# Kernel optimization log

Hardware: AMD Instinct MI355X
Metric: run time of the kernel (lower is better)

Reference implementation:

```python
import jax, jax.numpy as jnp
import numpy as np
import math

NHID = 256
QDIM = 256
T = 4096
B = 4

def setup_inputs() -> dict:
    key = jax.random.key(0)
    k1, k2, k3, k4 = jax.random.split(key, 4)
    # xavier_uniform with relu gain = sqrt(2)
    gain = math.sqrt(2.0)
    bound = gain * math.sqrt(6.0 / (NHID + QDIM))
    inputs = jax.random.normal(k1, (T, B, NHID), dtype=jnp.float32)
    W_q = jax.random.uniform(k2, (NHID, QDIM), minval=-bound, maxval=bound, dtype=jnp.float32)
    W_k = jax.random.uniform(k3, (NHID, QDIM), minval=-bound, maxval=bound, dtype=jnp.float32)
    W_v = jax.random.uniform(k4, (NHID, QDIM), minval=-bound, maxval=bound, dtype=jnp.float32)
    return {"inputs": inputs, "W_q": W_q, "W_k": W_k, "W_v": W_v}

def reference(inputs, W_q, W_k, W_v):
    # inputs: [T, B, H]. Original loops over time, recomputing attention of the
    # last token against the growing causal prefix. Step 0 emits x0 @ W_v, which
    # equals single-key softmax attention, so the whole thing is causal attention.
    scale = float(int(math.sqrt(QDIM)))  # faithful to int(math.sqrt(d)) in source
    q = jnp.einsum('tbh,hd->tbd', inputs, W_q)
    k = jnp.einsum('tbh,hd->tbd', inputs, W_k)
    v = jnp.einsum('tbh,hd->tbd', inputs, W_v)
    scores = jnp.einsum('ibd,jbd->bij', q, k) / scale  # [B, T, T]
    t = scores.shape[-1]
    causal = jnp.tril(jnp.ones((t, t), dtype=bool))
    scores = jnp.where(causal[None, :, :], scores, -jnp.inf)
    attn = jax.nn.softmax(scores, axis=-1)  # row i = attention_thru_time[i]
    results = jnp.einsum('bij,jbd->ibd', attn, v)  # [T, B, D]
    return results, attn
```

## Files before the change

### kernel.cpp

```cpp
#include <hip/hip_runtime.h>
#include <hip/hip_bf16.h>

#define T_DIM 4096
#define B_DIM 4

typedef unsigned short u16;
typedef __attribute__((ext_vector_type(4))) short s16x4;
typedef __attribute__((ext_vector_type(8))) short short8;
typedef __attribute__((ext_vector_type(8))) __bf16 bf16x8;
typedef __attribute__((ext_vector_type(4))) float f32x4;

static __device__ __forceinline__ u16 f2bf(float f) {
    union { float f; unsigned int u; } v; v.f = f;
    unsigned int u = v.u;
    u += 0x7FFFu + ((u >> 16) & 1u);
    return (u16)(u >> 16);
}

static __device__ __forceinline__ f32x4 mfma_k32(short8 a, short8 b, f32x4 c) {
    return __builtin_amdgcn_mfma_f32_16x16x32_bf16(
        __builtin_bit_cast(bf16x8, a), __builtin_bit_cast(bf16x8, b), c, 0, 0, 0);
}
static __device__ __forceinline__ f32x4 mfma_k16(s16x4 a, s16x4 b, f32x4 c) {
    return __builtin_amdgcn_mfma_f32_16x16x16bf16_1k(a, b, c, 0, 0, 0);
}

__global__ __launch_bounds__(256) void wtrans_kernel(
    const float* __restrict__ Wq, const float* __restrict__ Wk,
    const float* __restrict__ Wv, u16* __restrict__ wT) {
    int idx = blockIdx.x * 256 + threadIdx.x;
    int w   = idx >> 16;
    int rem = idx & 65535;
    int k   = rem >> 8;
    int n   = rem & 255;
    const float* W = (w == 0) ? Wq : (w == 1) ? Wk : Wv;
    wT[w * 65536 + n * 256 + k] = f2bf(W[k * 256 + n]);
}

__global__ __launch_bounds__(256, 4) void proj_kernel(
    const float* __restrict__ X, const u16* __restrict__ wT,
    u16* __restrict__ qf, u16* __restrict__ kf, u16* __restrict__ vfw) {
    const int r0  = blockIdx.x * 16;
    const int wid = threadIdx.x >> 6, lane = threadIdx.x & 63;
    const int lr  = lane & 15, lg = lane >> 4;

    short8 af[8];
    const float* xrow = X + (size_t)(r0 + lr) * 256 + lg * 8;
#pragma unroll
    for (int kc = 0; kc < 8; ++kc) {
        f32x4 xa = *(const f32x4*)(xrow + kc * 32);
        f32x4 xb = *(const f32x4*)(xrow + kc * 32 + 4);
        union { u16 u[8]; short8 v; } t;
#pragma unroll
        for (int e = 0; e < 4; ++e) { t.u[e] = f2bf(xa[e]); t.u[4 + e] = f2bf(xb[e]); }
        af[kc] = t.v;
    }

    for (int w = 0; w < 3; ++w) {
        f32x4 acc[4];
#pragma unroll
        for (int nf = 0; nf < 4; ++nf) acc[nf] = (f32x4){0.f,0.f,0.f,0.f};
        const u16* wbase = wT + w * 65536 + (size_t)(16 * (4 * wid) + lr) * 256 + lg * 8;
#pragma unroll
        for (int kc = 0; kc < 8; ++kc)
#pragma unroll
            for (int nf = 0; nf < 4; ++nf) {
                short8 bfv = *(const short8*)(wbase + nf * 16 * 256 + kc * 32);
                acc[nf] = mfma_k32(af[kc], bfv, acc[nf]);
            }
#pragma unroll
        for (int nf = 0; nf < 4; ++nf)
#pragma unroll
            for (int r = 0; r < 4; ++r) {
                int rg = r0 + 4 * lg + r;
                int t  = rg >> 2, bb = rg & 3;
                int d  = 16 * (4 * wid + nf) + lr;
                u16 val = f2bf(acc[nf][r]);
                if (w < 2) {
                    int tile = t >> 4, lrq = t & 15;
                    int kc = d >> 5, lgq = (d >> 3) & 3, e = d & 7;
                    size_t idx = ((((size_t)bb * 256 + tile) * 8 + kc) * 64
                                  + lrq + 16 * lgq) * 8 + e;
                    if (w == 0) qf[idx] = val; else kf[idx] = val;
                } else {
                    int jt = t >> 6, c = (t >> 4) & 3;
                    int cc = c >> 1, eh = c & 1;
                    int lgv = (t >> 2) & 3, el = t & 3, e = eh * 4 + el;
                    int nfv = d >> 4, lrv = d & 15;
                    size_t idx = (((((size_t)bb * 64 + jt) * 16 + nfv) * 2 + cc) * 64
                                  + lrv + 16 * lgv) * 8 + e;
                    vfw[idx] = val;
                }
            }
    }
}

__global__ __launch_bounds__(512) void attn_kernel(
    const u16* __restrict__ qf, const u16* __restrict__ kf,
    const u16* __restrict__ vfw, float* __restrict__ out) {
    __shared__ float l_sm[32];
    __shared__ float O_sm[32 * 264];

    const int blk = blockIdx.x;
    const int xcd = blk & 7;
    const int b = xcd >> 1, par = xcd & 1;
    const int pair = 2 * (blk >> 3) + par;

    const int tid = threadIdx.x;
    const int wid = tid >> 6, lane = tid & 63;
    const int f = wid >> 2, h = wid & 3;
    const int lr = lane & 15, lg = lane >> 4;

    float* attnO = out + (size_t)T_DIM * B_DIM * 256 + (size_t)b * T_DIM * T_DIM;

    for (int phase = 0; phase < 2; ++phase) {
        const int it = phase ? (127 - pair) : pair;
        const int i0 = it * 32;
        const int irow = i0 + 16 * f + lr;
        const int numJT = it / 2 + 1;

        __syncthreads();
        if (tid < 32) l_sm[tid] = 0.f;
        __syncthreads();

        short8 q8[8];
        const short8* qp = (const short8*)(qf + (((size_t)b * 256 + it * 2 + f) * 8) * 512);
#pragma unroll
        for (int kc = 0; kc < 8; ++kc) q8[kc] = qp[kc * 64 + lane];

        float rs = 0.f;
        for (int jt = 0; jt < numJT; ++jt) {
            const short8* kp = (const short8*)(kf + (((size_t)b * 256 + jt * 4 + h) * 8) * 512);
            f32x4 a = {0.f,0.f,0.f,0.f};
#pragma unroll
            for (int kc = 0; kc < 8; ++kc)
                a = mfma_k32(kp[kc * 64 + lane], q8[kc], a);
            const int j0 = jt * 64 + 16 * h + 4 * lg;
#pragma unroll
            for (int r = 0; r < 4; ++r)
                rs += (j0 + r <= irow) ? __expf(a[r] * 0.0625f) : 0.f;
        }
        rs += __shfl_xor(rs, 16, 64);
        rs += __shfl_xor(rs, 32, 64);
        if (lane < 16) atomicAdd(&l_sm[16 * f + lr], rs);
        __syncthreads();
        const float inv = 1.0f / l_sm[16 * f + lr];

        f32x4 oacc[16];
#pragma unroll
        for (int nf = 0; nf < 16; ++nf) oacc[nf] = (f32x4){0.f,0.f,0.f,0.f};

        for (int jt = 0; jt < numJT; ++jt) {
            const short8* kp = (const short8*)(kf + (((size_t)b * 256 + jt * 4 + h) * 8) * 512);
            f32x4 a = {0.f,0.f,0.f,0.f};
#pragma unroll
            for (int kc = 0; kc < 8; ++kc)
                a = mfma_k32(kp[kc * 64 + lane], q8[kc], a);

            const int j0 = jt * 64 + 16 * h + 4 * lg;
#pragma unroll
            for (int r = 0; r < 4; ++r)
                a[r] = (j0 + r <= irow) ? __expf(a[r] * 0.0625f) * inv : 0.f;
            __builtin_nontemporal_store(a,
                (f32x4*)(attnO + (size_t)irow * T_DIM + j0));

            union { u16 u[4]; s16x4 v; } t;
#pragma unroll
            for (int r = 0; r < 4; ++r) t.u[r] = f2bf(a[r]);
            const s16x4 pk = t.v;

            const u16* vb = vfw + (((size_t)b * 64 + jt) * 32 + (h >> 1)) * 512
                          + (size_t)lane * 8 + (h & 1) * 4;
#pragma unroll
            for (int nf = 0; nf < 16; ++nf) {
                s16x4 vf = *(const s16x4*)(vb + (size_t)nf * 1024);
                oacc[nf] = mfma_k16(pk, vf, oacc[nf]);
            }
        }

        for (int step = 0; step < 4; ++step) {
            if (h == step) {
#pragma unroll
                for (int nf = 0; nf < 16; ++nf)
#pragma unroll
                    for (int r = 0; r < 4; ++r) {
                        int row = 16 * f + 4 * lg + r, d = 16 * nf + lr;
                        if (step == 0) O_sm[row * 264 + d] = oacc[nf][r];
                        else           O_sm[row * 264 + d] += oacc[nf][r];
                    }
            }
            __syncthreads();
        }
#pragma unroll
        for (int u = 0; u < 4; ++u) {
            int ix = tid + 512 * u;
            int row = ix >> 6, c = ix & 63;
            f32x4 v = *(const f32x4*)(O_sm + row * 264 + c * 4);
            __builtin_nontemporal_store(v,
                (f32x4*)(out + ((size_t)(i0 + row) * B_DIM + b) * 256 + c * 4));
        }

        const int z0 = numJT * 64;
        if (z0 < T_DIM) {
            const int n4 = (T_DIM - z0) >> 2;
            for (int rr = 0; rr < 32; ++rr) {
                f32x4* rowp = (f32x4*)(attnO + (size_t)(i0 + rr) * T_DIM + z0);
                for (int c = tid; c < n4; c += 512) {
                    f32x4 z = {0.f, 0.f, 0.f, 0.f};
                    __builtin_nontemporal_store(z, rowp + c);
                }
            }
        }
    }
}

extern "C" void kernel_launch(void* const* d_in, const int* in_sizes, int n_in,
                              void* d_out, int out_size, void* d_ws, size_t ws_size,
                              hipStream_t stream) {
    (void)in_sizes; (void)n_in; (void)out_size; (void)ws_size;
    const float* X  = (const float*)d_in[0];
    const float* Wq = (const float*)d_in[1];
    const float* Wk = (const float*)d_in[2];
    const float* Wv = (const float*)d_in[3];
    float* out = (float*)d_out;

    char* ws = (char*)d_ws;
    u16* qf  = (u16*)(ws);
    u16* kf  = (u16*)(ws + (size_t)8  * 1024 * 1024);
    u16* vfw = (u16*)(ws + (size_t)16 * 1024 * 1024);
    u16* wT  = (u16*)(ws + (size_t)24 * 1024 * 1024);

    wtrans_kernel<<<dim3(768), dim3(256), 0, stream>>>(Wq, Wk, Wv, wT);
    proj_kernel<<<dim3(1024), dim3(256), 0, stream>>>(X, wT, qf, kf, vfw);
    attn_kernel<<<dim3(256), dim3(512), 0, stream>>>(qf, kf, vfw, out);
}
```

Measured before the change: 258.1 us.

## Split attention key tiles across two blocks and add a partial-output sum kernel

The attention kernel now launches twice as many blocks. Each pair of blocks splits the key tiles of a query tile by parity, and the zero-fill of the masked attention region is split between them too. Each block writes its partial output to a workspace buffer, and a new kernel adds the two partials into the final output layout. This is meant to raise parallelism and occupancy on the GPU. The cost is that both blocks still compute the full softmax denominator, plus extra global traffic for the partial buffers and one more launch.

```diff
diff --git a/kernel.cpp b/kernel.cpp
--- a/kernel.cpp
+++ b/kernel.cpp
@@ -95,16 +95,18 @@
     }
 }
 
-__global__ __launch_bounds__(512) void attn_kernel(
+__global__ __launch_bounds__(512) void attn_kernel2(
     const u16* __restrict__ qf, const u16* __restrict__ kf,
-    const u16* __restrict__ vfw, float* __restrict__ out) {
+    const u16* __restrict__ vfw, float* __restrict__ opart,
+    float* __restrict__ out) {
     __shared__ float l_sm[32];
     __shared__ float O_sm[32 * 264];
 
     const int blk = blockIdx.x;
     const int xcd = blk & 7;
-    const int b = xcd >> 1, par = xcd & 1;
-    const int pair = 2 * (blk >> 3) + par;
+    const int b = xcd >> 1;
+    const int s = blk & 1;
+    const int pair = blk >> 3;
 
     const int tid = threadIdx.x;
     const int wid = tid >> 6, lane = tid & 63;
@@ -150,7 +152,7 @@
 #pragma unroll
         for (int nf = 0; nf < 16; ++nf) oacc[nf] = (f32x4){0.f,0.f,0.f,0.f};
 
-        for (int jt = 0; jt < numJT; ++jt) {
+        for (int jt = s; jt < numJT; jt += 2) {
             const short8* kp = (const short8*)(kf + (((size_t)b * 256 + jt * 4 + h) * 8) * 512);
             f32x4 a = {0.f,0.f,0.f,0.f};
 #pragma unroll
@@ -191,13 +193,13 @@
             }
             __syncthreads();
         }
+        float* op = opart + ((size_t)s * B_DIM * T_DIM + (size_t)b * T_DIM + i0) * 256;
 #pragma unroll
         for (int u = 0; u < 4; ++u) {
             int ix = tid + 512 * u;
             int row = ix >> 6, c = ix & 63;
             f32x4 v = *(const f32x4*)(O_sm + row * 264 + c * 4);
-            __builtin_nontemporal_store(v,
-                (f32x4*)(out + ((size_t)(i0 + row) * B_DIM + b) * 256 + c * 4));
+            __builtin_nontemporal_store(v, (f32x4*)(op + (size_t)row * 256 + c * 4));
         }
 
         const int z0 = numJT * 64;
@@ -205,13 +207,27 @@
             const int n4 = (T_DIM - z0) >> 2;
             for (int rr = 0; rr < 32; ++rr) {
                 f32x4* rowp = (f32x4*)(attnO + (size_t)(i0 + rr) * T_DIM + z0);
-                for (int c = tid; c < n4; c += 512) {
+                for (int c = tid + s * 512; c < n4; c += 1024) {
                     f32x4 z = {0.f, 0.f, 0.f, 0.f};
                     __builtin_nontemporal_store(z, rowp + c);
                 }
             }
         }
     }
+}
+
+__global__ __launch_bounds__(256) void osum_kernel(
+    const float* __restrict__ opart, float* __restrict__ out) {
+    size_t idx = (size_t)(blockIdx.x * 256 + threadIdx.x) * 4;
+    size_t bt = idx >> 8;
+    size_t d  = idx & 255;
+    size_t b  = bt >> 12, t = bt & 4095;
+    f32x4 v0 = *(const f32x4*)(opart + (((size_t)0 * B_DIM + b) * T_DIM + t) * 256 + d);
+    f32x4 v1 = *(const f32x4*)(opart + (((size_t)1 * B_DIM + b) * T_DIM + t) * 256 + d);
+    f32x4 v;
+#pragma unroll
+    for (int e = 0; e < 4; ++e) v[e] = v0[e] + v1[e];
+    __builtin_nontemporal_store(v, (f32x4*)(out + (t * B_DIM + b) * 256 + d));
 }
 
 extern "C" void kernel_launch(void* const* d_in, const int* in_sizes, int n_in,
@@ -229,8 +245,10 @@
     u16* kf  = (u16*)(ws + (size_t)8  * 1024 * 1024);
     u16* vfw = (u16*)(ws + (size_t)16 * 1024 * 1024);
     u16* wT  = (u16*)(ws + (size_t)24 * 1024 * 1024);
+    float* opart = (float*)(ws + (size_t)25 * 1024 * 1024);
 
     wtrans_kernel<<<dim3(768), dim3(256), 0, stream>>>(Wq, Wk, Wv, wT);
     proj_kernel<<<dim3(1024), dim3(256), 0, stream>>>(X, wT, qf, kf, vfw);
-    attn_kernel<<<dim3(256), dim3(512), 0, stream>>>(qf, kf, vfw, out);
-}
+    attn_kernel2<<<dim3(512), dim3(512), 0, stream>>>(qf, kf, vfw, opart, out);
+    osum_kernel<<<dim3(4096), dim3(256), 0, stream>>>(opart, out);
+}
```

New measurement: 328.6 us. 1.27x slower.
